# Optimization experiments

Hardware: AMD Instinct MI355X
Metric: run time of the kernel (lower is better)

The kernel has to match this reference:

```python
import jax, jax.numpy as jnp
import numpy as np

# Module / input configuration
N, H, W, C = 4, 64, 64, 128
G = 4                    # groups
GC = C // G              # group_channels = 32 (power of 2)
KS = 3                   # kernel_size (also dw_kernel_size)
P = KS * KS              # sampling points per group
STRIDE, PAD, DIL = 1, 1, 1
OFFSET_SCALE = 1.0
LN_EPS = 1e-6
DW_PAD = (KS - 1) // 2


def dcnv3_core(x, offset, mask):
    """DCNv3 sampling core (matches _C.dcnv3_forward / InternImage pytorch core).
    x: (N,H,W,C) projected input; offset: (N,Ho,Wo,G*P*2); mask: (N,Ho,Wo,G*P)."""
    n, h, w, _ = x.shape
    xp = jnp.pad(x, ((0, 0), (PAD, PAD), (PAD, PAD), (0, 0)))
    H_in, W_in = h + 2 * PAD, w + 2 * PAD
    Ho = (H_in - (DIL * (KS - 1) + 1)) // STRIDE + 1
    Wo = (W_in - (DIL * (KS - 1) + 1)) // STRIDE + 1
    # reference points in normalized padded coords (align_corners=False convention)
    base = (DIL * (KS - 1)) // 2 + 0.5
    ref_x = (base + jnp.arange(Wo, dtype=x.dtype) * STRIDE) / W_in
    ref_y = (base + jnp.arange(Ho, dtype=x.dtype) * STRIDE) / H_in
    rx, ry = jnp.broadcast_arrays(ref_x[None, :], ref_y[:, None])
    ref = jnp.stack([rx, ry], -1)                      # (Ho,Wo,2), (x,y)
    # dilation grid, w-index-major ordering as in reference impl
    gx = (jnp.arange(KS, dtype=x.dtype) * DIL - (DIL * (KS - 1)) // 2) / W_in
    gy = (jnp.arange(KS, dtype=x.dtype) * DIL - (DIL * (KS - 1)) // 2) / H_in
    gxm, gym = jnp.meshgrid(gx, gy, indexing='ij')
    grid = jnp.stack([gxm, gym], -1).reshape(P, 2)     # (P,2)
    norm = jnp.array([W_in, H_in], x.dtype)
    loc = (ref[None, :, :, None, None, :]
           + grid[None, None, None, None, :, :] * OFFSET_SCALE
           + offset.reshape(n, Ho, Wo, G, P, 2) * OFFSET_SCALE / norm)
    # normalized -> pixel coords (grid_sample align_corners=False): p = loc*size - 0.5
    px = loc[..., 0] * W_in - 0.5                      # (N,Ho,Wo,G,P)
    py = loc[..., 1] * H_in - 0.5
    xg = xp.reshape(n, H_in, W_in, G, GC)
    x0 = jnp.floor(px)
    y0 = jnp.floor(py)
    bi = jnp.arange(n).reshape(n, 1, 1, 1, 1)
    gi = jnp.arange(G).reshape(1, 1, 1, G, 1)

    def gather(iy, ix):
        valid = (ix >= 0) & (ix < W_in) & (iy >= 0) & (iy < H_in)
        ixc = jnp.clip(ix, 0, W_in - 1).astype(jnp.int32)
        iyc = jnp.clip(iy, 0, H_in - 1).astype(jnp.int32)
        v = xg[bi, iyc, ixc, gi]                       # (N,Ho,Wo,G,P,GC)
        return jnp.where(valid[..., None], v, jnp.zeros((), x.dtype))

    wx1 = px - x0
    wy1 = py - y0
    wx0 = 1.0 - wx1
    wy0 = 1.0 - wy1
    val = (gather(y0, x0) * (wy0 * wx0)[..., None]
           + gather(y0, x0 + 1) * (wy0 * wx1)[..., None]
           + gather(y0 + 1, x0) * (wy1 * wx0)[..., None]
           + gather(y0 + 1, x0 + 1) * (wy1 * wx1)[..., None])
    out = (val * mask.reshape(n, Ho, Wo, G, P, 1)).sum(4)   # (N,Ho,Wo,G,GC)
    return out.reshape(n, Ho, Wo, G * GC)


def setup_inputs() -> dict:
    key = jax.random.key(0)
    ks = jax.random.split(key, 8)
    s = lambda fan: 1.0 / np.sqrt(fan)
    return {
        'input': jax.random.normal(ks[0], (N, H, W, C), jnp.float32),
        'w_in': jax.random.normal(ks[1], (C, C), jnp.float32) * s(C),
        'b_in': jnp.zeros((C,), jnp.float32),
        'w_out': jax.random.normal(ks[2], (C, C), jnp.float32) * s(C),
        'b_out': jnp.zeros((C,), jnp.float32),
        'w_off': jax.random.normal(ks[3], (C, G * P * 2), jnp.float32) * 0.01,
        'b_off': jnp.zeros((G * P * 2,), jnp.float32),
        'w_mask': jax.random.normal(ks[4], (C, G * P), jnp.float32) * 0.01,
        'b_mask': jnp.zeros((G * P,), jnp.float32),
        'dw_kernel': jax.random.normal(ks[5], (KS, KS, 1, C), jnp.float32) * s(KS * KS),
        'dw_bias': jnp.zeros((C,), jnp.float32),
        'ln_gamma': jnp.ones((C,), jnp.float32),
        'ln_beta': jnp.zeros((C,), jnp.float32),
    }


def reference(input, w_in, b_in, w_out, b_out, w_off, b_off, w_mask, b_mask,
              dw_kernel, dw_bias, ln_gamma, ln_beta):
    # input_proj
    x = input @ w_in + b_in
    # dw_conv branch: depthwise conv -> LayerNorm (channels_last, eps=1e-6) -> GELU (exact)
    x1 = jax.lax.conv_general_dilated(
        input, dw_kernel, (1, 1), [(DW_PAD, DW_PAD), (DW_PAD, DW_PAD)],
        feature_group_count=C,
        dimension_numbers=('NHWC', 'HWIO', 'NHWC')) + dw_bias
    mu = x1.mean(-1, keepdims=True)
    var = ((x1 - mu) ** 2).mean(-1, keepdims=True)
    x1 = (x1 - mu) * jax.lax.rsqrt(var + LN_EPS) * ln_gamma + ln_beta
    x1 = jax.nn.gelu(x1, approximate=False)
    # offsets and softmax-normalized modulation mask
    offset = x1 @ w_off + b_off
    mask = jax.nn.softmax((x1 @ w_mask + b_mask).reshape(N, H, W, G, P), axis=-1)
    mask = mask.reshape(N, H, W, G * P)
    # deformable sampling core
    x = dcnv3_core(x, offset, mask)
    # output_proj
    return x @ w_out + b_out
```

## Files before the change

### kernel.cpp

```cpp
#include <hip/hip_runtime.h>
#include <math.h>

#define NB 4
#define HH 64
#define WW 64
#define CC 128
#define GG 4
#define GC 32
#define PP 9
#define MPIX (NB*HH*WW)
#define PIXC ((size_t)MPIX*CC)

typedef short bf16x8 __attribute__((ext_vector_type(8)));
typedef float f32x4  __attribute__((ext_vector_type(4)));

__device__ __forceinline__ ushort f2bf(float f) {
    uint u = __float_as_uint(f);
    u += 0x7FFFu + ((u >> 16) & 1u);
    return (ushort)(u >> 16);
}
__device__ __forceinline__ float bf2f(ushort h) {
    return __uint_as_float(((uint)h) << 16);
}

__global__ __launch_bounds__(256) void prep_weights(
    const float* __restrict__ w_in, const float* __restrict__ w_out,
    const float* __restrict__ w_off, const float* __restrict__ b_off,
    const float* __restrict__ w_mask, const float* __restrict__ b_mask,
    ushort* __restrict__ BT, float* __restrict__ bpack)
{
    int idx = blockIdx.x * 256 + threadIdx.x;
    if (idx < 3 * 128 * 32) {
        int m  = idx >> 12;
        int r  = idx & 4095;
        int n  = r >> 5;
        int k4 = (r & 31) << 2;
        ushort h[4], l[4];
#pragma unroll
        for (int j = 0; j < 4; j++) {
            int k = k4 + j;
            float a;
            if (m == 0)      a = w_in[k * 128 + n];
            else if (m == 2) a = w_out[k * 128 + n];
            else             a = (n < 72) ? w_off[k * 72 + n]
                               : (n < 108 ? w_mask[k * 36 + (n - 72)] : 0.f);
            ushort hh = f2bf(a);
            h[j] = hh;
            l[j] = f2bf(a - bf2f(hh));
        }
        ushort* dh = BT + m * 32768 + n * 128 + k4;
        ushort* dl = dh + 16384;
        *(ushort4*)dh = make_ushort4(h[0], h[1], h[2], h[3]);
        *(ushort4*)dl = make_ushort4(l[0], l[1], l[2], l[3]);
    } else if (idx < 3 * 128 * 32 + 128) {
        int n = idx - 3 * 128 * 32;
        bpack[n] = (n < 72) ? b_off[n] : (n < 108 ? b_mask[n - 72] : 0.f);
    }
}

__global__ __launch_bounds__(256) void gemm_mfma(
    const float* __restrict__ A, const ushort* __restrict__ BTh,
    const ushort* __restrict__ BTl, const float* __restrict__ bias,
    float* __restrict__ C)
{
    __shared__ ushort sB[2][128][128];

    const int t = threadIdx.x;

#pragma unroll
    for (int i = 0; i < 16; i++) {
        int c    = i * 256 + t;
        int part = c >> 11;
        int rem  = c & 2047;
        int n    = rem >> 4;
        int kc   = (rem & 15) << 3;
        const ushort* src = (part ? BTl : BTh) + n * 128 + kc;
        int4 v = *(const int4*)src;
        int byte = part * 32768 + n * 256 + ((kc * 2) ^ ((n & 7) << 4));
        *(int4*)((char*)sB + byte) = v;
    }
    __syncthreads();

    const int w  = t >> 6;
    const int l  = t & 63;
    const int lr = l & 15;
    const int lk = l >> 4;
    const int row0 = (blockIdx.x << 6) + (w << 4);
    const float* Arow = A + (size_t)(row0 + lr) * 128;

    f32x4 acc[8];
#pragma unroll
    for (int nt = 0; nt < 8; nt++) acc[nt] = (f32x4){0.f, 0.f, 0.f, 0.f};

#pragma unroll
    for (int ks = 0; ks < 4; ks++) {
        const float4 a0 = *(const float4*)(Arow + ks * 32 + lk * 8);
        const float4 a1 = *(const float4*)(Arow + ks * 32 + lk * 8 + 4);
        float av[8] = {a0.x, a0.y, a0.z, a0.w, a1.x, a1.y, a1.z, a1.w};
        bf16x8 ah, al;
#pragma unroll
        for (int j = 0; j < 8; j++) {
            ushort hh = f2bf(av[j]);
            ah[j] = (short)hh;
            al[j] = (short)f2bf(av[j] - bf2f(hh));
        }
        bf16x8 bh[8], bl[8];
#pragma unroll
        for (int nt = 0; nt < 8; nt++) {
            int n = nt * 16 + lr;
            int byte = n * 256 + (((ks * 32 + lk * 8) * 2) ^ ((n & 7) << 4));
            bh[nt] = *(const bf16x8*)((const char*)sB + byte);
            bl[nt] = *(const bf16x8*)((const char*)sB + 32768 + byte);
        }
#pragma unroll
        for (int nt = 0; nt < 8; nt++)
            acc[nt] = __builtin_amdgcn_mfma_f32_16x16x32_bf16(ah, bh[nt], acc[nt], 0, 0, 0);
#pragma unroll
        for (int nt = 0; nt < 8; nt++)
            acc[nt] = __builtin_amdgcn_mfma_f32_16x16x32_bf16(al, bh[nt], acc[nt], 0, 0, 0);
#pragma unroll
        for (int nt = 0; nt < 8; nt++)
            acc[nt] = __builtin_amdgcn_mfma_f32_16x16x32_bf16(ah, bl[nt], acc[nt], 0, 0, 0);
    }

#pragma unroll
    for (int nt = 0; nt < 8; nt++) {
        int col = nt * 16 + lr;
        float bv = bias[col];
#pragma unroll
        for (int i = 0; i < 4; i++)
            C[(size_t)(row0 + lk * 4 + i) * 128 + col] = acc[nt][i] + bv;
    }
}

__global__ __launch_bounds__(256) void dw_ln_gelu(
    const float* __restrict__ x, const float* __restrict__ kern,
    const float* __restrict__ kbias, const float* __restrict__ gamma,
    const float* __restrict__ beta, float* __restrict__ y)
{
    const int t  = threadIdx.x;
    const int pl = t >> 5;
    const int cq = (t & 31) << 2;
    const int pix = blockIdx.x * 8 + pl;
    const int w = pix & 63;
    const int h = (pix >> 6) & 63;
    const int b = pix >> 12;

    float4 acc = make_float4(0.f, 0.f, 0.f, 0.f);
#pragma unroll
    for (int kh = 0; kh < 3; kh++) {
        int hy = h + kh - 1;
        if (hy < 0 || hy > 63) continue;
#pragma unroll
        for (int kw = 0; kw < 3; kw++) {
            int wx = w + kw - 1;
            if (wx < 0 || wx > 63) continue;
            const float4 v  = *(const float4*)(x + (((size_t)((b * 64 + hy) * 64 + wx)) << 7) + cq);
            const float4 kv = *(const float4*)(kern + ((kh * 3 + kw) << 7) + cq);
            acc.x = fmaf(v.x, kv.x, acc.x);
            acc.y = fmaf(v.y, kv.y, acc.y);
            acc.z = fmaf(v.z, kv.z, acc.z);
            acc.w = fmaf(v.w, kv.w, acc.w);
        }
    }
    const float4 kb = *(const float4*)(kbias + cq);
    acc.x += kb.x; acc.y += kb.y; acc.z += kb.z; acc.w += kb.w;

    float s  = acc.x + acc.y + acc.z + acc.w;
    float s2 = acc.x * acc.x + acc.y * acc.y + acc.z * acc.z + acc.w * acc.w;
#pragma unroll
    for (int m = 16; m >= 1; m >>= 1) {
        s  += __shfl_xor(s, m);
        s2 += __shfl_xor(s2, m);
    }
    const float mu   = s * (1.f / 128.f);
    const float var  = s2 * (1.f / 128.f) - mu * mu;
    const float rstd = 1.f / sqrtf(var + 1e-6f);

    const float4 g  = *(const float4*)(gamma + cq);
    const float4 bb = *(const float4*)(beta + cq);
    float vv[4] = {acc.x, acc.y, acc.z, acc.w};
    float gg[4] = {g.x, g.y, g.z, g.w};
    float be[4] = {bb.x, bb.y, bb.z, bb.w};
    float4 outv;
    float* po = &outv.x;
#pragma unroll
    for (int i = 0; i < 4; i++) {
        float xh = (vv[i] - mu) * rstd * gg[i] + be[i];
        po[i] = 0.5f * xh * (1.f + erff(xh * 0.70710678118654752f));
    }
    *(float4*)(y + ((size_t)pix << 7) + cq) = outv;
}

__global__ __launch_bounds__(256) void dcn_sample(
    const float* __restrict__ xp, const float* __restrict__ om,
    float* __restrict__ out)
{
    const int t = threadIdx.x;
    const int q = t & 3;
    const int g = (t >> 2) & 3;
    const int pix = blockIdx.x * 16 + (t >> 4);
    const int w = pix & 63;
    const int h = (pix >> 6) & 63;
    const int b = pix >> 12;

    const float* ompix = om + ((size_t)pix << 7);

    float lg[9];
    float mx = -1e30f;
#pragma unroll
    for (int p = 0; p < 9; p++) {
        lg[p] = ompix[72 + g * 9 + p];
        mx = fmaxf(mx, lg[p]);
    }
    float sum = 0.f;
#pragma unroll
    for (int p = 0; p < 9; p++) { lg[p] = expf(lg[p] - mx); sum += lg[p]; }
    const float inv = 1.f / sum;

    float4 acc0 = make_float4(0.f, 0.f, 0.f, 0.f);
    float4 acc1 = make_float4(0.f, 0.f, 0.f, 0.f);
    const int chbase = g * 32 + q * 8;

#pragma unroll
    for (int p = 0; p < 9; p++) {
        const float ox = ompix[g * 18 + 2 * p];
        const float oy = ompix[g * 18 + 2 * p + 1];
        const float px = (float)(w + p / 3 - 1) + ox;
        const float py = (float)(h + p % 3 - 1) + oy;
        const float fx0 = floorf(px), fy0 = floorf(py);
        const int x0 = (int)fx0, y0 = (int)fy0;
        const float wx1 = px - fx0, wy1 = py - fy0;
        const float wx0 = 1.f - wx1, wy0 = 1.f - wy1;
        const float m = lg[p] * inv;
        const float cw[4] = {wy0 * wx0 * m, wy0 * wx1 * m, wy1 * wx0 * m, wy1 * wx1 * m};
        const int cx[4] = {x0, x0 + 1, x0, x0 + 1};
        const int cy[4] = {y0, y0, y0 + 1, y0 + 1};
#pragma unroll
        for (int c = 0; c < 4; c++) {
            const int xx = cx[c], yy = cy[c];
            if (xx >= 0 && xx < 64 && yy >= 0 && yy < 64) {
                const float* src = xp + (((size_t)((b * 64 + yy) * 64 + xx)) << 7) + chbase;
                const float4 v0 = *(const float4*)(src);
                const float4 v1 = *(const float4*)(src + 4);
                const float wt = cw[c];
                acc0.x = fmaf(v0.x, wt, acc0.x); acc0.y = fmaf(v0.y, wt, acc0.y);
                acc0.z = fmaf(v0.z, wt, acc0.z); acc0.w = fmaf(v0.w, wt, acc0.w);
                acc1.x = fmaf(v1.x, wt, acc1.x); acc1.y = fmaf(v1.y, wt, acc1.y);
                acc1.z = fmaf(v1.z, wt, acc1.z); acc1.w = fmaf(v1.w, wt, acc1.w);
            }
        }
    }
    float* dst = out + ((size_t)pix << 7) + chbase;
    *(float4*)(dst)     = acc0;
    *(float4*)(dst + 4) = acc1;
}

extern "C" void kernel_launch(void* const* d_in, const int* in_sizes, int n_in,
                              void* d_out, int out_size, void* d_ws, size_t ws_size,
                              hipStream_t stream)
{
    const float* input   = (const float*)d_in[0];
    const float* w_in    = (const float*)d_in[1];
    const float* b_in    = (const float*)d_in[2];
    const float* w_out   = (const float*)d_in[3];
    const float* b_out   = (const float*)d_in[4];
    const float* w_off   = (const float*)d_in[5];
    const float* b_off   = (const float*)d_in[6];
    const float* w_mask  = (const float*)d_in[7];
    const float* b_mask  = (const float*)d_in[8];
    const float* dw_kern = (const float*)d_in[9];
    const float* dw_bias = (const float*)d_in[10];
    const float* ln_g    = (const float*)d_in[11];
    const float* ln_b    = (const float*)d_in[12];
    float* out = (float*)d_out;

    float* ws      = (float*)d_ws;
    float* x_proj  = ws;
    float* x1      = ws + PIXC;
    float* offmask = ws + 2 * PIXC;
    ushort* BT     = (ushort*)(ws + 3 * PIXC);
    float* bpack   = (float*)(BT + 3 * 32768);
    float* sampled = x1;

    prep_weights<<<49, 256, 0, stream>>>(w_in, w_out, w_off, b_off, w_mask, b_mask,
                                         BT, bpack);
    gemm_mfma<<<MPIX / 64, 256, 0, stream>>>(input, BT, BT + 16384, b_in, x_proj);
    dw_ln_gelu<<<MPIX / 8, 256, 0, stream>>>(input, dw_kern, dw_bias, ln_g, ln_b, x1);
    gemm_mfma<<<MPIX / 64, 256, 0, stream>>>(x1, BT + 32768, BT + 49152, bpack, offmask);
    dcn_sample<<<MPIX / 16, 256, 0, stream>>>(x_proj, offmask, sampled);
    gemm_mfma<<<MPIX / 64, 256, 0, stream>>>(sampled, BT + 65536, BT + 81920, b_out, out);
}
```

Before: 134.5 us.

## Fuse dwconv-LN-GELU and DCN sampling into their following MFMA GEMMs

Fuses the depthwise conv/LayerNorm/GELU stage with the offset/mask GEMM, and the deformable sampling stage with the output projection GEMM. The A operand is now split into bf16 hi/lo in LDS and B fragments are held in registers, each wave covering 32 output columns. This removes the x1 and sampled intermediate round trips to global memory and two launches. In exchange it uses smaller per-block tiles (32 or 16 rows), and each block reloads its B fragments from global memory.

```diff
diff --git a/kernel.cpp b/kernel.cpp
--- a/kernel.cpp
+++ b/kernel.cpp
@@ -11,8 +11,10 @@
 #define MPIX (NB*HH*WW)
 #define PIXC ((size_t)MPIX*CC)
 
-typedef short bf16x8 __attribute__((ext_vector_type(8)));
-typedef float f32x4  __attribute__((ext_vector_type(4)));
+typedef short  bf16x8 __attribute__((ext_vector_type(8)));
+typedef ushort u16x8  __attribute__((ext_vector_type(8)));
+typedef ushort u16x4  __attribute__((ext_vector_type(4)));
+typedef float  f32x4  __attribute__((ext_vector_type(4)));
 
 __device__ __forceinline__ ushort f2bf(float f) {
     uint u = __float_as_uint(f);
@@ -58,148 +60,198 @@
     }
 }
 
-__global__ __launch_bounds__(256) void gemm_mfma(
+template<int MT>
+__device__ __forceinline__ void gemm_tail_lds(
+    const ushort* __restrict__ BTh, const ushort* __restrict__ BTl,
+    const float* __restrict__ bias, float* __restrict__ C,
+    int row0, const char* sA)
+{
+    const int t  = threadIdx.x;
+    const int wv = t >> 6;
+    const int l  = t & 63;
+    const int lr = l & 15;
+    const int lk = l >> 4;
+    const int planeBytes = MT * 16 * 256;
+
+    bf16x8 bh[2][4], bl[2][4];
+#pragma unroll
+    for (int nt = 0; nt < 2; nt++) {
+        const int n = wv * 32 + nt * 16 + lr;
+#pragma unroll
+        for (int ks = 0; ks < 4; ks++) {
+            const int o = n * 128 + ks * 32 + lk * 8;
+            bh[nt][ks] = *(const bf16x8*)(BTh + o);
+            bl[nt][ks] = *(const bf16x8*)(BTl + o);
+        }
+    }
+
+    f32x4 acc[MT][2];
+#pragma unroll
+    for (int m = 0; m < MT; m++) {
+        acc[m][0] = (f32x4){0.f, 0.f, 0.f, 0.f};
+        acc[m][1] = (f32x4){0.f, 0.f, 0.f, 0.f};
+    }
+
+#pragma unroll
+    for (int ks = 0; ks < 4; ks++) {
+        bf16x8 ah[MT], al[MT];
+#pragma unroll
+        for (int m = 0; m < MT; m++) {
+            const int row = m * 16 + lr;
+            const int off = row * 256 + ((((ks * 32 + lk * 8) * 2)) ^ ((row & 7) << 4));
+            ah[m] = *(const bf16x8*)(sA + off);
+            al[m] = *(const bf16x8*)(sA + planeBytes + off);
+        }
+#pragma unroll
+        for (int m = 0; m < MT; m++) {
+            acc[m][0] = __builtin_amdgcn_mfma_f32_16x16x32_bf16(ah[m], bh[0][ks], acc[m][0], 0, 0, 0);
+            acc[m][1] = __builtin_amdgcn_mfma_f32_16x16x32_bf16(ah[m], bh[1][ks], acc[m][1], 0, 0, 0);
+        }
+#pragma unroll
+        for (int m = 0; m < MT; m++) {
+            acc[m][0] = __builtin_amdgcn_mfma_f32_16x16x32_bf16(al[m], bh[0][ks], acc[m][0], 0, 0, 0);
+            acc[m][1] = __builtin_amdgcn_mfma_f32_16x16x32_bf16(al[m], bh[1][ks], acc[m][1], 0, 0, 0);
+        }
+#pragma unroll
+        for (int m = 0; m < MT; m++) {
+            acc[m][0] = __builtin_amdgcn_mfma_f32_16x16x32_bf16(ah[m], bl[0][ks], acc[m][0], 0, 0, 0);
+            acc[m][1] = __builtin_amdgcn_mfma_f32_16x16x32_bf16(ah[m], bl[1][ks], acc[m][1], 0, 0, 0);
+        }
+    }
+
+#pragma unroll
+    for (int m = 0; m < MT; m++) {
+#pragma unroll
+        for (int nt = 0; nt < 2; nt++) {
+            const int col = wv * 32 + nt * 16 + lr;
+            const float bv = bias[col];
+#pragma unroll
+            for (int i = 0; i < 4; i++)
+                C[(size_t)(row0 + m * 16 + lk * 4 + i) * 128 + col] = acc[m][nt][i] + bv;
+        }
+    }
+}
+
+__global__ __launch_bounds__(256) void k1_inproj(
     const float* __restrict__ A, const ushort* __restrict__ BTh,
     const ushort* __restrict__ BTl, const float* __restrict__ bias,
     float* __restrict__ C)
 {
-    __shared__ ushort sB[2][128][128];
-
+    __shared__ __align__(16) char sA[2 * 32 * 256];
     const int t = threadIdx.x;
-
-#pragma unroll
-    for (int i = 0; i < 16; i++) {
-        int c    = i * 256 + t;
-        int part = c >> 11;
-        int rem  = c & 2047;
-        int n    = rem >> 4;
-        int kc   = (rem & 15) << 3;
-        const ushort* src = (part ? BTl : BTh) + n * 128 + kc;
-        int4 v = *(const int4*)src;
-        int byte = part * 32768 + n * 256 + ((kc * 2) ^ ((n & 7) << 4));
-        *(int4*)((char*)sB + byte) = v;
+    const int row0 = blockIdx.x * 32;
+
+    const int row = t >> 3;
+    const int ch0 = (t & 7) * 16;
+    const float* src = A + (size_t)(row0 + row) * 128 + ch0;
+    float f[16];
+#pragma unroll
+    for (int j = 0; j < 4; j++)
+        *(float4*)(f + j * 4) = *(const float4*)(src + j * 4);
+#pragma unroll
+    for (int c = 0; c < 2; c++) {
+        u16x8 hv, lv;
+#pragma unroll
+        for (int j = 0; j < 8; j++) {
+            const float v = f[c * 8 + j];
+            const ushort hh = f2bf(v);
+            hv[j] = hh;
+            lv[j] = f2bf(v - bf2f(hh));
+        }
+        const int byte = row * 256 + (((ch0 + c * 8) * 2) ^ ((row & 7) << 4));
+        *(u16x8*)(sA + byte) = hv;
+        *(u16x8*)(sA + 32 * 256 + byte) = lv;
     }
     __syncthreads();
-
-    const int w  = t >> 6;
-    const int l  = t & 63;
-    const int lr = l & 15;
-    const int lk = l >> 4;
-    const int row0 = (blockIdx.x << 6) + (w << 4);
-    const float* Arow = A + (size_t)(row0 + lr) * 128;
-
-    f32x4 acc[8];
-#pragma unroll
-    for (int nt = 0; nt < 8; nt++) acc[nt] = (f32x4){0.f, 0.f, 0.f, 0.f};
-
-#pragma unroll
-    for (int ks = 0; ks < 4; ks++) {
-        const float4 a0 = *(const float4*)(Arow + ks * 32 + lk * 8);
-        const float4 a1 = *(const float4*)(Arow + ks * 32 + lk * 8 + 4);
-        float av[8] = {a0.x, a0.y, a0.z, a0.w, a1.x, a1.y, a1.z, a1.w};
-        bf16x8 ah, al;
-#pragma unroll
-        for (int j = 0; j < 8; j++) {
-            ushort hh = f2bf(av[j]);
-            ah[j] = (short)hh;
-            al[j] = (short)f2bf(av[j] - bf2f(hh));
-        }
-        bf16x8 bh[8], bl[8];
-#pragma unroll
-        for (int nt = 0; nt < 8; nt++) {
-            int n = nt * 16 + lr;
-            int byte = n * 256 + (((ks * 32 + lk * 8) * 2) ^ ((n & 7) << 4));
-            bh[nt] = *(const bf16x8*)((const char*)sB + byte);
-            bl[nt] = *(const bf16x8*)((const char*)sB + 32768 + byte);
-        }
-#pragma unroll
-        for (int nt = 0; nt < 8; nt++)
-            acc[nt] = __builtin_amdgcn_mfma_f32_16x16x32_bf16(ah, bh[nt], acc[nt], 0, 0, 0);
-#pragma unroll
-        for (int nt = 0; nt < 8; nt++)
-            acc[nt] = __builtin_amdgcn_mfma_f32_16x16x32_bf16(al, bh[nt], acc[nt], 0, 0, 0);
-#pragma unroll
-        for (int nt = 0; nt < 8; nt++)
-            acc[nt] = __builtin_amdgcn_mfma_f32_16x16x32_bf16(ah, bl[nt], acc[nt], 0, 0, 0);
-    }
-
-#pragma unroll
-    for (int nt = 0; nt < 8; nt++) {
-        int col = nt * 16 + lr;
-        float bv = bias[col];
-#pragma unroll
-        for (int i = 0; i < 4; i++)
-            C[(size_t)(row0 + lk * 4 + i) * 128 + col] = acc[nt][i] + bv;
-    }
-}
-
-__global__ __launch_bounds__(256) void dw_ln_gelu(
+    gemm_tail_lds<2>(BTh, BTl, bias, C, row0, sA);
+}
+
+__global__ __launch_bounds__(256) void k2_dwln_off(
     const float* __restrict__ x, const float* __restrict__ kern,
     const float* __restrict__ kbias, const float* __restrict__ gamma,
-    const float* __restrict__ beta, float* __restrict__ y)
-{
+    const float* __restrict__ beta, const ushort* __restrict__ BTh,
+    const ushort* __restrict__ BTl, const float* __restrict__ bias,
+    float* __restrict__ C)
+{
+    __shared__ __align__(16) char sA[2 * 32 * 256];
     const int t  = threadIdx.x;
     const int pl = t >> 5;
     const int cq = (t & 31) << 2;
-    const int pix = blockIdx.x * 8 + pl;
-    const int w = pix & 63;
-    const int h = (pix >> 6) & 63;
-    const int b = pix >> 12;
-
-    float4 acc = make_float4(0.f, 0.f, 0.f, 0.f);
-#pragma unroll
-    for (int kh = 0; kh < 3; kh++) {
-        int hy = h + kh - 1;
-        if (hy < 0 || hy > 63) continue;
-#pragma unroll
-        for (int kw = 0; kw < 3; kw++) {
-            int wx = w + kw - 1;
-            if (wx < 0 || wx > 63) continue;
-            const float4 v  = *(const float4*)(x + (((size_t)((b * 64 + hy) * 64 + wx)) << 7) + cq);
-            const float4 kv = *(const float4*)(kern + ((kh * 3 + kw) << 7) + cq);
-            acc.x = fmaf(v.x, kv.x, acc.x);
-            acc.y = fmaf(v.y, kv.y, acc.y);
-            acc.z = fmaf(v.z, kv.z, acc.z);
-            acc.w = fmaf(v.w, kv.w, acc.w);
-        }
-    }
-    const float4 kb = *(const float4*)(kbias + cq);
-    acc.x += kb.x; acc.y += kb.y; acc.z += kb.z; acc.w += kb.w;
-
-    float s  = acc.x + acc.y + acc.z + acc.w;
-    float s2 = acc.x * acc.x + acc.y * acc.y + acc.z * acc.z + acc.w * acc.w;
-#pragma unroll
-    for (int m = 16; m >= 1; m >>= 1) {
-        s  += __shfl_xor(s, m);
-        s2 += __shfl_xor(s2, m);
-    }
-    const float mu   = s * (1.f / 128.f);
-    const float var  = s2 * (1.f / 128.f) - mu * mu;
-    const float rstd = 1.f / sqrtf(var + 1e-6f);
-
-    const float4 g  = *(const float4*)(gamma + cq);
-    const float4 bb = *(const float4*)(beta + cq);
-    float vv[4] = {acc.x, acc.y, acc.z, acc.w};
-    float gg[4] = {g.x, g.y, g.z, g.w};
-    float be[4] = {bb.x, bb.y, bb.z, bb.w};
-    float4 outv;
-    float* po = &outv.x;
-#pragma unroll
-    for (int i = 0; i < 4; i++) {
-        float xh = (vv[i] - mu) * rstd * gg[i] + be[i];
-        po[i] = 0.5f * xh * (1.f + erff(xh * 0.70710678118654752f));
-    }
-    *(float4*)(y + ((size_t)pix << 7) + cq) = outv;
-}
-
-__global__ __launch_bounds__(256) void dcn_sample(
+    const int pix0 = blockIdx.x * 32;
+
+#pragma unroll
+    for (int pass = 0; pass < 4; pass++) {
+        const int lpix = pass * 8 + pl;
+        const int pix  = pix0 + lpix;
+        const int w = pix & 63;
+        const int h = (pix >> 6) & 63;
+        const int b = pix >> 12;
+
+        float4 acc = make_float4(0.f, 0.f, 0.f, 0.f);
+#pragma unroll
+        for (int kh = 0; kh < 3; kh++) {
+            const int hy = h + kh - 1;
+            if (hy < 0 || hy > 63) continue;
+#pragma unroll
+            for (int kw = 0; kw < 3; kw++) {
+                const int wx = w + kw - 1;
+                if (wx < 0 || wx > 63) continue;
+                const float4 v  = *(const float4*)(x + (((size_t)((b * 64 + hy) * 64 + wx)) << 7) + cq);
+                const float4 kv = *(const float4*)(kern + ((kh * 3 + kw) << 7) + cq);
+                acc.x = fmaf(v.x, kv.x, acc.x);
+                acc.y = fmaf(v.y, kv.y, acc.y);
+                acc.z = fmaf(v.z, kv.z, acc.z);
+                acc.w = fmaf(v.w, kv.w, acc.w);
+            }
+        }
+        const float4 kb = *(const float4*)(kbias + cq);
+        acc.x += kb.x; acc.y += kb.y; acc.z += kb.z; acc.w += kb.w;
+
+        float s  = acc.x + acc.y + acc.z + acc.w;
+        float s2 = acc.x * acc.x + acc.y * acc.y + acc.z * acc.z + acc.w * acc.w;
+#pragma unroll
+        for (int m = 16; m >= 1; m >>= 1) {
+            s  += __shfl_xor(s, m);
+            s2 += __shfl_xor(s2, m);
+        }
+        const float mu   = s * (1.f / 128.f);
+        const float var  = s2 * (1.f / 128.f) - mu * mu;
+        const float rstd = 1.f / sqrtf(var + 1e-6f);
+
+        const float4 g  = *(const float4*)(gamma + cq);
+        const float4 bb = *(const float4*)(beta + cq);
+        const float vv[4] = {acc.x, acc.y, acc.z, acc.w};
+        const float gg[4] = {g.x, g.y, g.z, g.w};
+        const float be[4] = {bb.x, bb.y, bb.z, bb.w};
+        u16x4 hv, lv;
+#pragma unroll
+        for (int i = 0; i < 4; i++) {
+            const float xh = (vv[i] - mu) * rstd * gg[i] + be[i];
+            const float gl = 0.5f * xh * (1.f + erff(xh * 0.70710678118654752f));
+            const ushort hh = f2bf(gl);
+            hv[i] = hh;
+            lv[i] = f2bf(gl - bf2f(hh));
+        }
+        const int byte = lpix * 256 + ((cq * 2) ^ ((lpix & 7) << 4));
+        *(u16x4*)(sA + byte) = hv;
+        *(u16x4*)(sA + 32 * 256 + byte) = lv;
+    }
+    __syncthreads();
+    gemm_tail_lds<2>(BTh, BTl, bias, C, pix0, sA);
+}
+
+__global__ __launch_bounds__(256) void k3_sample_out(
     const float* __restrict__ xp, const float* __restrict__ om,
-    float* __restrict__ out)
-{
+    const ushort* __restrict__ BTh, const ushort* __restrict__ BTl,
+    const float* __restrict__ bias, float* __restrict__ out)
+{
+    __shared__ __align__(16) char sA[2 * 16 * 256];
     const int t = threadIdx.x;
     const int q = t & 3;
     const int g = (t >> 2) & 3;
-    const int pix = blockIdx.x * 16 + (t >> 4);
+    const int lpix = t >> 4;
+    const int pix0 = blockIdx.x * 16;
+    const int pix = pix0 + lpix;
     const int w = pix & 63;
     const int h = (pix >> 6) & 63;
     const int b = pix >> 12;
@@ -251,9 +303,20 @@
             }
         }
     }
-    float* dst = out + ((size_t)pix << 7) + chbase;
-    *(float4*)(dst)     = acc0;
-    *(float4*)(dst + 4) = acc1;
+
+    const float sv[8] = {acc0.x, acc0.y, acc0.z, acc0.w, acc1.x, acc1.y, acc1.z, acc1.w};
+    u16x8 hv, lv;
+#pragma unroll
+    for (int j = 0; j < 8; j++) {
+        const ushort hh = f2bf(sv[j]);
+        hv[j] = hh;
+        lv[j] = f2bf(sv[j] - bf2f(hh));
+    }
+    const int byte = lpix * 256 + ((chbase * 2) ^ ((lpix & 7) << 4));
+    *(u16x8*)(sA + byte) = hv;
+    *(u16x8*)(sA + 16 * 256 + byte) = lv;
+    __syncthreads();
+    gemm_tail_lds<1>(BTh, BTl, bias, out, pix0, sA);
 }
 
 extern "C" void kernel_launch(void* const* d_in, const int* in_sizes, int n_in,
@@ -277,17 +340,15 @@
 
     float* ws      = (float*)d_ws;
     float* x_proj  = ws;
-    float* x1      = ws + PIXC;
-    float* offmask = ws + 2 * PIXC;
-    ushort* BT     = (ushort*)(ws + 3 * PIXC);
+    float* offmask = ws + PIXC;
+    ushort* BT     = (ushort*)(ws + 2 * PIXC);
     float* bpack   = (float*)(BT + 3 * 32768);
-    float* sampled = x1;
 
     prep_weights<<<49, 256, 0, stream>>>(w_in, w_out, w_off, b_off, w_mask, b_mask,
                                          BT, bpack);
-    gemm_mfma<<<MPIX / 64, 256, 0, stream>>>(input, BT, BT + 16384, b_in, x_proj);
-    dw_ln_gelu<<<MPIX / 8, 256, 0, stream>>>(input, dw_kern, dw_bias, ln_g, ln_b, x1);
-    gemm_mfma<<<MPIX / 64, 256, 0, stream>>>(x1, BT + 32768, BT + 49152, bpack, offmask);
-    dcn_sample<<<MPIX / 16, 256, 0, stream>>>(x_proj, offmask, sampled);
-    gemm_mfma<<<MPIX / 64, 256, 0, stream>>>(sampled, BT + 65536, BT + 81920, b_out, out);
-}
+    k1_inproj<<<MPIX / 32, 256, 0, stream>>>(input, BT, BT + 16384, b_in, x_proj);
+    k2_dwln_off<<<MPIX / 32, 256, 0, stream>>>(input, dw_kern, dw_bias, ln_g, ln_b,
+                                               BT + 32768, BT + 49152, bpack, offmask);
+    k3_sample_out<<<MPIX / 16, 256, 0, stream>>>(x_proj, offmask,
+                                                 BT + 65536, BT + 81920, b_out, out);
+}
```

After: 136.0 us. No clear change (+1.1%).
